# Performance work log

Measured on AMD Instinct MI355X. Metric: run time of the kernel, lower is better.

Reference implementation:

```python
import jax, jax.numpy as jnp
import numpy as np

B, D, E, K = 2048, 768, 8, 2   # tokens, d_model, num_experts, top-k
H = 4 * D                       # FeedForward hidden = 4 * n_embed
LOSS_COEF = 1e-2


def setup_inputs() -> dict:
    key = jax.random.key(0)
    ks = jax.random.split(key, 5)
    s = 0.02
    return {
        "x": jax.random.normal(ks[0], (B, D), jnp.float32),
        "w_gate": jax.random.normal(ks[1], (D, E), jnp.float32) * s,
        "W1": jax.random.normal(ks[2], (E, D, H), jnp.float32) * s,
        "b1": jnp.zeros((E, H), jnp.float32),
        "W2": jax.random.normal(ks[3], (E, H, D), jnp.float32) * s,
        "b2": jnp.zeros((E, D), jnp.float32),
    }


def _cv_squared(v):
    # torch .var() is unbiased (ddof=1)
    eps = 1e-10
    return v.var(ddof=1) / (v.mean() ** 2 + eps)


def reference(x, w_gate, W1, b1, W2, b2):
    # --- noisy_top_k_gating with train=False (clean logits, no noise) ---
    logits = x @ w_gate                                   # [B, E]
    top_vals, top_idx = jax.lax.top_k(logits, K)          # [B, K]
    top_gates = jax.nn.softmax(top_vals, axis=1)          # softmax over the k selected logits
    rows = jnp.arange(x.shape[0])[:, None]
    gates = jnp.zeros_like(logits).at[rows, top_idx].set(top_gates)  # scatter into [B, E]

    importance = gates.sum(0)                             # [E]
    load = (gates > 0).sum(0).astype(jnp.float32)         # [E] (_gates_to_load)
    loss = (_cv_squared(importance) + _cv_squared(load)) * LOSS_COEF

    # --- expert FFNs (dense over experts; gates zero out non-selected) ---
    # equivalent math to SparseDispatcher dispatch/compute/combine:
    # y[b] = sum_e gates[b,e] * FFN_e(x[b])
    h = jax.nn.gelu(jnp.einsum('bd,edh->ebh', x, W1) + b1[:, None, :], approximate=False)  # [E,B,H]
    out = jnp.einsum('ebh,ehd->ebd', h, W2) + b2[:, None, :]                               # [E,B,D]
    y = jnp.einsum('be,ebd->bd', gates, out)                                               # [B,D]
    return y, loss
```

## Files before the change

kernel.cpp:

```cpp
#include <hip/hip_runtime.h>
#include <math.h>

#define Btok 2048
#define Dm   768
#define NE   8
#define Hh   3072
#define OBROWS 5120

typedef short short8 __attribute__((ext_vector_type(8)));
typedef float f32x4  __attribute__((ext_vector_type(4)));

__device__ __forceinline__ short f2bf(float f) {
    unsigned u = __builtin_bit_cast(unsigned, f);
    u += 0x7fffu + ((u >> 16) & 1u);
    return (short)(u >> 16);
}

__device__ __forceinline__ float gelu_exact(float v) {
    return 0.5f * v * (1.0f + erff(v * 0.70710678118654752440f));
}

#define GLDS(gsrc, ldst)                                                           \
    __builtin_amdgcn_global_load_lds(                                              \
        (const __attribute__((address_space(1))) void*)(gsrc),                     \
        (__attribute__((address_space(3))) void*)(ldst),                           \
        16, 0, 0)

__device__ __forceinline__ void logits_body(const float* __restrict__ x,
                                            const float* __restrict__ wg,
                                            int* __restrict__ t2e,
                                            float* __restrict__ tokgate,
                                            unsigned short* __restrict__ xb,
                                            int b) {
    int wv   = threadIdx.x >> 6;
    int lane = threadIdx.x & 63;
    int tok  = b * 4 + wv;

    const float* xr = x + (size_t)tok * Dm;
    float xv[12];
#pragma unroll
    for (int i = 0; i < 12; ++i) xv[i] = xr[lane + i * 64];

    unsigned short* xw = xb + (size_t)tok * Dm;
#pragma unroll
    for (int i = 0; i < 12; ++i) xw[lane + i * 64] = (unsigned short)f2bf(xv[i]);

    float acc[NE];
#pragma unroll
    for (int e = 0; e < NE; ++e) acc[e] = 0.f;
#pragma unroll
    for (int i = 0; i < 12; ++i) {
        int d = lane + i * 64;
#pragma unroll
        for (int e = 0; e < NE; ++e) acc[e] += xv[i] * wg[d * NE + e];
    }
#pragma unroll
    for (int e = 0; e < NE; ++e) {
#pragma unroll
        for (int off = 32; off > 0; off >>= 1) acc[e] += __shfl_xor(acc[e], off);
    }

    if (lane == 0) {
        int i0 = 0; float v0 = acc[0];
#pragma unroll
        for (int e = 1; e < NE; ++e) { if (acc[e] > v0) { v0 = acc[e]; i0 = e; } }
        int i1 = -1; float v1 = -1e30f;
#pragma unroll
        for (int e = 0; e < NE; ++e) {
            if (e == i0) continue;
            if (acc[e] > v1) { v1 = acc[e]; i1 = e; }
        }
        float tt = __expf(v1 - v0);
        float g0 = 1.0f / (1.0f + tt);
        float g1 = 1.0f - g0;

        t2e[tok * 2 + 0]     = i0;
        t2e[tok * 2 + 1]     = i1;
        tokgate[tok * 2 + 0] = g0;
        tokgate[tok * 2 + 1] = g1;
    }
}

__device__ __forceinline__ void transpose_body(float (*tile)[65],
                                               const float* __restrict__ in,
                                               unsigned short* __restrict__ out,
                                               int ldIn, int ldOut,
                                               size_t eStrideIn, size_t eStrideOut,
                                               int rowOff, int colOff,
                                               int bx, int by, int bz) {
    const float* src = in + (size_t)bz * eStrideIn
                     + (size_t)(rowOff + by * 64) * ldIn + colOff + bx * 64;
    unsigned short* dst = out + (size_t)bz * eStrideOut
                        + (size_t)(bx * 64) * ldOut + by * 64;
    int t = threadIdx.x;
    int r = t >> 4, c4 = (t & 15) * 4;
#pragma unroll
    for (int it = 0; it < 4; ++it) {
        float4 v = *(const float4*)(src + (size_t)(it * 16 + r) * ldIn + c4);
        tile[it * 16 + r][c4 + 0] = v.x;
        tile[it * 16 + r][c4 + 1] = v.y;
        tile[it * 16 + r][c4 + 2] = v.z;
        tile[it * 16 + r][c4 + 3] = v.w;
    }
    __syncthreads();
#pragma unroll
    for (int it = 0; it < 4; ++it) {
        int n = it * 16 + r;
        unsigned short o0 = (unsigned short)f2bf(tile[c4 + 0][n]);
        unsigned short o1 = (unsigned short)f2bf(tile[c4 + 1][n]);
        unsigned short o2 = (unsigned short)f2bf(tile[c4 + 2][n]);
        unsigned short o3 = (unsigned short)f2bf(tile[c4 + 3][n]);
        uint2 o;
        o.x = (unsigned)o0 | ((unsigned)o1 << 16);
        o.y = (unsigned)o2 | ((unsigned)o3 << 16);
        *(uint2*)(dst + (size_t)n * ldOut + c4) = o;
    }
}

__global__ __launch_bounds__(256)
void transpose_kernel(const float* __restrict__ in, unsigned short* __restrict__ out,
                      int ldIn, int ldOut, size_t eStrideIn, size_t eStrideOut,
                      int rowOff, int colOff) {
    __shared__ float tile[64][65];
    transpose_body(tile, in, out, ldIn, ldOut, eStrideIn, eStrideOut, rowOff, colOff,
                   blockIdx.x, blockIdx.y, blockIdx.z);
}

__global__ __launch_bounds__(256)
void prep_kernel(const float* __restrict__ x,
                 const float* __restrict__ wg,
                 int* __restrict__ t2e,
                 float* __restrict__ tokgate,
                 unsigned short* __restrict__ xb,
                 const float* __restrict__ W1, unsigned short* __restrict__ w1t,
                 int Hc, int colBase) {
    __shared__ float tile[64][65];
    int b = blockIdx.x;
    const int NL = Btok / 4;

    if (b < NL) {
        logits_body(x, wg, t2e, tokgate, xb, b);
    } else {
        int nx1 = Hc / 64, ny1 = Dm / 64;
        int q  = b - NL;
        int bx = q % nx1; q /= nx1;
        int by = q % ny1;
        int bz = q / ny1;
        transpose_body(tile, W1, w1t, Hh, Dm, (size_t)Dm * Hh, (size_t)Hc * Dm,
                       0, colBase, bx, by, bz);
    }
}

__global__ __launch_bounds__(1024)
void assign_kernel(const int* __restrict__ t2e,
                   const float* __restrict__ tokgate,
                   int* __restrict__ padded,
                   int* __restrict__ offsets,
                   int* __restrict__ list,
                   int* __restrict__ tokes,
                   float* __restrict__ loss_out) {
    __shared__ int   scnt[NE];
    __shared__ int   spad[NE];
    __shared__ float simp[NE];
    int tid = threadIdx.x;
    if (tid < NE) { scnt[tid] = 0; simp[tid] = 0.f; }
    __syncthreads();

#pragma unroll
    for (int it = 0; it < Btok / 1024; ++it) {
        int tok = tid + it * 1024;
        int e0 = t2e[tok * 2], e1 = t2e[tok * 2 + 1];
        float g0 = tokgate[tok * 2], g1 = tokgate[tok * 2 + 1];
        int s0 = atomicAdd(&scnt[e0], 1);
        int s1 = atomicAdd(&scnt[e1], 1);
        list[e0 * Btok + s0] = tok;
        list[e1 * Btok + s1] = tok;
        tokes[tok * 2 + 0] = (e0 << 13) | s0;
        tokes[tok * 2 + 1] = (e1 << 13) | s1;
        atomicAdd(&simp[e0], g0);
        atomicAdd(&simp[e1], g1);
    }
    __syncthreads();

    if (tid == 0) {
        int off = 0;
        for (int e = 0; e < NE; ++e) {
            int p = (scnt[e] + 127) & ~127;
            spad[e]    = p;
            padded[e]  = p;
            offsets[e] = off;
            off += p;
        }
        float mi = 0.f, ml = 0.f;
        for (int e = 0; e < NE; ++e) { mi += simp[e]; ml += (float)scnt[e]; }
        mi *= (1.0f / NE); ml *= (1.0f / NE);
        float vi = 0.f, vl = 0.f;
        for (int e = 0; e < NE; ++e) {
            float di = simp[e] - mi;        vi += di * di;
            float dl = (float)scnt[e] - ml; vl += dl * dl;
        }
        vi /= (NE - 1); vl /= (NE - 1);
        loss_out[0] = 1e-2f * (vi / (mi * mi + 1e-10f) + vl / (ml * ml + 1e-10f));
    }
    __syncthreads();

    for (int e = 0; e < NE; ++e) {
        int c = scnt[e], p = spad[e];
        for (int s = c + tid; s < p; s += 1024) list[e * Btok + s] = 0;
    }
}

__global__ __launch_bounds__(256)
void gemm1_kernel(const unsigned short* __restrict__ xb,
                  const unsigned short* __restrict__ w1t,
                  const float* __restrict__ b1,
                  const int* __restrict__ list,
                  const int* __restrict__ padded,
                  const int* __restrict__ offsets,
                  unsigned short* __restrict__ hbuf,
                  int Hc, int colBase, int nG1, int nT2,
                  const float* __restrict__ W2,
                  unsigned short* __restrict__ w2t) {
    __shared__ union __align__(16) {
        struct { unsigned short As[2][4096]; unsigned short Bs[2][4096]; } g;
        float tile[64][65];
    } sm;

    int b = blockIdx.x;
    int gid;
    if (nT2 > 0) {
        int q = b / 5, r = b % 5;
        if (r >= 2) {
            int tix = q * 3 + (r - 2);
            int nx2 = Dm / 64, ny2 = Hc / 64;
            int bx = tix % nx2; tix /= nx2;
            int by = tix % ny2;
            int bz = tix / ny2;
            transpose_body(sm.tile, W2, w2t, Dm, Hc, (size_t)Hh * Dm, (size_t)Dm * Hc,
                           0, 0, bx, by, bz);
            return;
        }
        gid = q * 2 + r;
    } else {
        gid = b;
    }

    int NTQ = Hc / 128;
    int nt = gid % NTQ;
    int mt = (gid / NTQ) % 16;
    int e  = gid / (NTQ * 16);
    if (mt * 128 >= padded[e]) return;
    int roff = offsets[e];

    int t = threadIdx.x, w = t >> 6, lane = t & 63;
    int lr = lane & 15, lh = lane >> 4;
    int wr = (w >> 1) * 64, wc = (w & 1) * 64;
    int r0 = t >> 2;
    int ce = ((t & 3) ^ ((r0 >> 1) & 3)) * 8;
    int ks = (lh ^ ((lr >> 1) & 3)) * 8;

    const int* lst = list + e * Btok + mt * 128;
    int tok0 = lst[r0], tok1 = lst[64 + r0];
    const unsigned short* pa0 = xb + (size_t)tok0 * Dm + ce;
    const unsigned short* pa1 = xb + (size_t)tok1 * Dm + ce;
    const unsigned short* wbp = w1t + ((size_t)e * Hc + (size_t)nt * 128) * Dm;
    const unsigned short* pb0 = wbp + (size_t)r0 * Dm + ce;
    const unsigned short* pb1 = wbp + (size_t)(64 + r0) * Dm + ce;

    int s0 = __builtin_amdgcn_readfirstlane(w * 1024);

    f32x4 acc[4][4];
#pragma unroll
    for (int i = 0; i < 4; ++i)
#pragma unroll
        for (int j = 0; j < 4; ++j) acc[i][j] = (f32x4){0.f, 0.f, 0.f, 0.f};

    auto stage = [&](int buf, int kb) {
        GLDS(pa0 + kb, (char*)&sm.g.As[buf][0] + s0);
        GLDS(pa1 + kb, (char*)&sm.g.As[buf][0] + s0 + 4096);
        GLDS(pb0 + kb, (char*)&sm.g.Bs[buf][0] + s0);
        GLDS(pb1 + kb, (char*)&sm.g.Bs[buf][0] + s0 + 4096);
    };
    auto compute = [&](int buf) {
        short8 a[4], bq[4];
#pragma unroll
        for (int i = 0; i < 4; ++i) a[i] = *(const short8*)&sm.g.As[buf][(wr + i * 16 + lr) * 32 + ks];
#pragma unroll
        for (int j = 0; j < 4; ++j) bq[j] = *(const short8*)&sm.g.Bs[buf][(wc + j * 16 + lr) * 32 + ks];
#pragma unroll
        for (int i = 0; i < 4; ++i)
#pragma unroll
            for (int j = 0; j < 4; ++j)
                acc[i][j] = __builtin_amdgcn_mfma_f32_16x16x32_bf16(a[i], bq[j], acc[i][j], 0, 0, 0);
    };

    const int NTK = Dm / 32;
    stage(0, 0);
    __syncthreads();
    int cur = 0;
    for (int kt = 0; kt < NTK; ++kt) {
        if (kt + 1 < NTK) stage(cur ^ 1, (kt + 1) * 32);
        compute(cur);
        __syncthreads();
        cur ^= 1;
    }

    float bj[4];
#pragma unroll
    for (int j = 0; j < 4; ++j)
        bj[j] = b1[(size_t)e * Hh + colBase + nt * 128 + wc + j * 16 + lr];
#pragma unroll
    for (int i = 0; i < 4; ++i) {
#pragma unroll
        for (int j = 0; j < 4; ++j) {
#pragma unroll
            for (int r = 0; r < 4; ++r) {
                int row = wr + i * 16 + lh * 4 + r;
                float v = acc[i][j][r] + bj[j];
                v = gelu_exact(v);
                hbuf[(size_t)(roff + mt * 128 + row) * Hc + nt * 128 + wc + j * 16 + lr]
                    = (unsigned short)f2bf(v);
            }
        }
    }
}

__global__ __launch_bounds__(256)
void gemm2_kernel(const unsigned short* __restrict__ hbuf,
                  const unsigned short* __restrict__ w2t,
                  const int* __restrict__ padded,
                  const int* __restrict__ offsets,
                  float* __restrict__ obuf,
                  int Hc, int MT, int accum) {
    int id = blockIdx.x;
    int e  = id & 7;
    int rr = id >> 3;
    int mt = rr % MT; rr /= MT;
    int nt = rr % 6;
    int sk = rr / 6;
    if (mt * 128 >= padded[e]) return;
    int roff = offsets[e];
    int Kc = Hc >> 1, K0 = sk * Kc;

    __shared__ unsigned short As[2][4096];
    __shared__ unsigned short Bs[2][4096];

    int t = threadIdx.x, w = t >> 6, lane = t & 63;
    int lr = lane & 15, lh = lane >> 4;
    int wr = (w >> 1) * 64, wc = (w & 1) * 64;
    int r0 = t >> 2;
    int ce = ((t & 3) ^ ((r0 >> 1) & 3)) * 8;
    int ks = (lh ^ ((lr >> 1) & 3)) * 8;

    const unsigned short* ab  = hbuf + (size_t)(roff + mt * 128) * Hc + K0;
    const unsigned short* pa0 = ab + (size_t)r0 * Hc + ce;
    const unsigned short* pa1 = ab + (size_t)(64 + r0) * Hc + ce;
    const unsigned short* wbp = w2t + ((size_t)e * Dm + (size_t)nt * 128) * Hc + K0;
    const unsigned short* pb0 = wbp + (size_t)r0 * Hc + ce;
    const unsigned short* pb1 = wbp + (size_t)(64 + r0) * Hc + ce;

    int s0 = __builtin_amdgcn_readfirstlane(w * 1024);

    f32x4 acc[4][4];
#pragma unroll
    for (int i = 0; i < 4; ++i)
#pragma unroll
        for (int j = 0; j < 4; ++j) acc[i][j] = (f32x4){0.f, 0.f, 0.f, 0.f};

    auto stage = [&](int buf, int kb) {
        GLDS(pa0 + kb, (char*)&As[buf][0] + s0);
        GLDS(pa1 + kb, (char*)&As[buf][0] + s0 + 4096);
        GLDS(pb0 + kb, (char*)&Bs[buf][0] + s0);
        GLDS(pb1 + kb, (char*)&Bs[buf][0] + s0 + 4096);
    };
    auto compute = [&](int buf) {
        short8 a[4], bq[4];
#pragma unroll
        for (int i = 0; i < 4; ++i) a[i] = *(const short8*)&As[buf][(wr + i * 16 + lr) * 32 + ks];
#pragma unroll
        for (int j = 0; j < 4; ++j) bq[j] = *(const short8*)&Bs[buf][(wc + j * 16 + lr) * 32 + ks];
#pragma unroll
        for (int i = 0; i < 4; ++i)
#pragma unroll
            for (int j = 0; j < 4; ++j)
                acc[i][j] = __builtin_amdgcn_mfma_f32_16x16x32_bf16(a[i], bq[j], acc[i][j], 0, 0, 0);
    };

    const int NTK = Kc / 32;
    stage(0, 0);
    __syncthreads();
    int cur = 0;
    for (int kt = 0; kt < NTK; ++kt) {
        if (kt + 1 < NTK) stage(cur ^ 1, (kt + 1) * 32);
        compute(cur);
        __syncthreads();
        cur ^= 1;
    }

    float* orow = obuf + (size_t)sk * OBROWS * Dm
                + (size_t)(roff + mt * 128) * Dm + nt * 128;
#pragma unroll
    for (int i = 0; i < 4; ++i) {
#pragma unroll
        for (int r = 0; r < 4; ++r) {
            int row = wr + i * 16 + lh * 4 + r;
#pragma unroll
            for (int j = 0; j < 4; ++j) {
                int col = wc + j * 16 + lr;
                float v = acc[i][j][r];
                if (accum) v += orow[(size_t)row * Dm + col];
                orow[(size_t)row * Dm + col] = v;
            }
        }
    }
}

__global__ __launch_bounds__(256)
void combine_kernel(const float* __restrict__ obuf,
                    const int* __restrict__ offsets,
                    const int* __restrict__ tokes,
                    const float* __restrict__ tokgate,
                    const float* __restrict__ b2,
                    float* __restrict__ y) {
    int wv = threadIdx.x >> 6, lane = threadIdx.x & 63;
    int tok = blockIdx.x * 4 + wv;
    int p0 = tokes[tok * 2], p1 = tokes[tok * 2 + 1];
    float g0 = tokgate[tok * 2], g1 = tokgate[tok * 2 + 1];
    int e0 = p0 >> 13, ss0 = p0 & 8191;
    int e1 = p1 >> 13, ss1 = p1 & 8191;
    size_t r0 = (size_t)(offsets[e0] + ss0) * Dm;
    size_t r1 = (size_t)(offsets[e1] + ss1) * Dm;
    const size_t SLAB = (size_t)OBROWS * Dm;
#pragma unroll
    for (int i = 0; i < 3; ++i) {
        int col = (lane + i * 64) * 4;
        float4 a0 = *(const float4*)(obuf + r0 + col);
        float4 a1 = *(const float4*)(obuf + SLAB + r0 + col);
        float4 c0 = *(const float4*)(obuf + r1 + col);
        float4 c1 = *(const float4*)(obuf + SLAB + r1 + col);
        float4 be0 = *(const float4*)(b2 + (size_t)e0 * Dm + col);
        float4 be1 = *(const float4*)(b2 + (size_t)e1 * Dm + col);
        float4 o;
        o.x = g0 * (a0.x + a1.x + be0.x) + g1 * (c0.x + c1.x + be1.x);
        o.y = g0 * (a0.y + a1.y + be0.y) + g1 * (c0.y + c1.y + be1.y);
        o.z = g0 * (a0.z + a1.z + be0.z) + g1 * (c0.z + c1.z + be1.z);
        o.w = g0 * (a0.w + a1.w + be0.w) + g1 * (c0.w + c1.w + be1.w);
        *(float4*)(y + (size_t)tok * Dm + col) = o;
    }
}

extern "C" void kernel_launch(void* const* d_in, const int* in_sizes, int n_in,
                              void* d_out, int out_size, void* d_ws, size_t ws_size,
                              hipStream_t stream) {
    const float* x  = (const float*)d_in[0];
    const float* wg = (const float*)d_in[1];
    const float* W1 = (const float*)d_in[2];
    const float* b1 = (const float*)d_in[3];
    const float* W2 = (const float*)d_in[4];
    const float* b2 = (const float*)d_in[5];
    float* y = (float*)d_out;

    char* ws = (char*)d_ws;
    int*   padded     = (int*)(ws + 32);
    int*   offsets    = (int*)(ws + 64);
    int*   list       = (int*)(ws + 1024);
    int*   tokes      = (int*)(ws + 132096);
    float* tokgate    = (float*)(ws + 148480);
    int*   t2e        = (int*)(ws + 164864);
    unsigned short* xb = (unsigned short*)(ws + 262144);

    size_t base = (size_t)4 << 20;
    size_t osz  = (size_t)2 * OBROWS * Dm * sizeof(float);
    int C = 8;
    size_t wsz = 0, hsz = 0;
    for (int c = 1; c <= 8; c <<= 1) {
        wsz = (size_t)NE * (Hh / c) * Dm * 2;
        hsz = (size_t)OBROWS * (Hh / c) * 2;
        size_t need = base + 2 * wsz + hsz + ((c == 1) ? 0 : osz);
        C = c;
        if (need <= ws_size) break;
    }
    int Hc = Hh / C;
    wsz = (size_t)NE * Hc * Dm * 2;
    hsz = (size_t)OBROWS * Hc * 2;
    unsigned short* w1t  = (unsigned short*)(ws + base);
    unsigned short* w2t  = (unsigned short*)(ws + base + wsz);
    unsigned short* hbuf = (unsigned short*)(ws + base + 2 * wsz);
    float* obuf = (C == 1) ? (float*)w1t : (float*)(ws + base + 2 * wsz + hsz);

    const int MT = 16;
    int nT1 = (Hc / 64) * (Dm / 64) * NE;
    int nT2 = (Dm / 64) * (Hc / 64) * NE;
    int nG1 = (Hc / 128) * MT * NE;

    prep_kernel<<<Btok / 4 + nT1, 256, 0, stream>>>(
        x, wg, t2e, tokgate, xb, W1, w1t, Hc, 0);
    assign_kernel<<<1, 1024, 0, stream>>>(t2e, tokgate, padded, offsets, list, tokes,
                                          y + (size_t)Btok * Dm);

    for (int c = 0; c < C; ++c) {
        if (c > 0) {
            transpose_kernel<<<dim3(Hc / 64, Dm / 64, NE), 256, 0, stream>>>(
                W1, w1t, Hh, Dm, (size_t)Dm * Hh, (size_t)Hc * Dm, 0, c * Hc);
            transpose_kernel<<<dim3(Dm / 64, Hc / 64, NE), 256, 0, stream>>>(
                W2, w2t, Dm, Hc, (size_t)Hh * Dm, (size_t)Dm * Hc, c * Hc, 0);
        }
        int extra = (c == 0) ? nT2 : 0;
        gemm1_kernel<<<nG1 + extra, 256, 0, stream>>>(
            xb, w1t, b1, list, padded, offsets, hbuf, Hc, c * Hc, nG1, extra, W2, w2t);
        gemm2_kernel<<<8 * MT * 6 * 2, 256, 0, stream>>>(
            hbuf, w2t, padded, offsets, obuf, Hc, MT, (c == 0) ? 0 : 1);
    }
    combine_kernel<<<Btok / 4, 256, 0, stream>>>(obuf, offsets, tokes, tokgate, b2, y);
}
```

Baseline: 137.1 us.

## Compact active GEMM1 tiles and balance W2 transposes through an atomic queue

The assign kernel now builds a compact table of the non-empty (expert, row-tile) pairs and a tile count. GEMM1 blocks index into that table instead of mapping onto a fixed 16-tiles-per-expert grid, so blocks are no longer spent on tiles that immediately exit. The fused W2 transpose work is no longer statically given to 3 of every 5 blocks. Every block, including those that finish their GEMM tile, pulls transpose tiles from an atomic counter, which balances transpose work against GEMM work. The cost is an atomic plus two barriers per transpose tile, and the grid is now sized to nG1 with half its blocks doing only transposes in the first chunk.

Result: slower. 201.2 us (+46.7%).

```diff
diff --git a/kernel.cpp b/kernel.cpp
--- a/kernel.cpp
+++ b/kernel.cpp
@@ -158,7 +158,10 @@
                    int* __restrict__ offsets,
                    int* __restrict__ list,
                    int* __restrict__ tokes,
-                   float* __restrict__ loss_out) {
+                   float* __restrict__ loss_out,
+                   int* __restrict__ tbl,
+                   int* __restrict__ ntile,
+                   int* __restrict__ tq) {
     __shared__ int   scnt[NE];
     __shared__ int   spad[NE];
     __shared__ float simp[NE];
@@ -184,13 +187,17 @@
 
     if (tid == 0) {
         int off = 0;
+        int n = 0;
         for (int e = 0; e < NE; ++e) {
             int p = (scnt[e] + 127) & ~127;
             spad[e]    = p;
             padded[e]  = p;
             offsets[e] = off;
             off += p;
-        }
+            for (int mt = 0; mt * 128 < p; ++mt) tbl[n++] = (e << 8) | mt;
+        }
+        ntile[0] = n;
+        tq[0]    = 0;
         float mi = 0.f, ml = 0.f;
         for (int e = 0; e < NE; ++e) { mi += simp[e]; ml += (float)scnt[e]; }
         mi *= (1.0f / NE); ml *= (1.0f / NE);
@@ -215,112 +222,125 @@
                   const unsigned short* __restrict__ w1t,
                   const float* __restrict__ b1,
                   const int* __restrict__ list,
-                  const int* __restrict__ padded,
                   const int* __restrict__ offsets,
+                  const int* __restrict__ tbl,
+                  const int* __restrict__ ntile,
                   unsigned short* __restrict__ hbuf,
-                  int Hc, int colBase, int nG1, int nT2,
+                  int Hc, int colBase, int nT2,
                   const float* __restrict__ W2,
-                  unsigned short* __restrict__ w2t) {
+                  unsigned short* __restrict__ w2t,
+                  int* __restrict__ tq) {
     __shared__ union __align__(16) {
         struct { unsigned short As[2][4096]; unsigned short Bs[2][4096]; } g;
         float tile[64][65];
     } sm;
-
-    int b = blockIdx.x;
+    __shared__ int curT;
+
+    int bid = blockIdx.x;
     int gid;
     if (nT2 > 0) {
-        int q = b / 5, r = b % 5;
-        if (r >= 2) {
-            int tix = q * 3 + (r - 2);
-            int nx2 = Dm / 64, ny2 = Hc / 64;
-            int bx = tix % nx2; tix /= nx2;
-            int by = tix % ny2;
-            int bz = tix / ny2;
+        int q = bid >> 2, r = bid & 3;
+        gid = (r < 2) ? (q * 2 + r) : -1;
+    } else {
+        gid = bid;
+    }
+
+    int NTQ  = Hc / 128;
+    int nAct = ntile[0];
+
+    if (gid >= 0 && gid < nAct * NTQ) {
+        int nt = gid % NTQ;
+        int pk = tbl[gid / NTQ];
+        int e  = pk >> 8;
+        int mt = pk & 255;
+        int roff = offsets[e];
+
+        int t = threadIdx.x, w = t >> 6, lane = t & 63;
+        int lr = lane & 15, lh = lane >> 4;
+        int wr = (w >> 1) * 64, wc = (w & 1) * 64;
+        int r0 = t >> 2;
+        int ce = ((t & 3) ^ ((r0 >> 1) & 3)) * 8;
+        int ks = (lh ^ ((lr >> 1) & 3)) * 8;
+
+        const int* lst = list + e * Btok + mt * 128;
+        int tok0 = lst[r0], tok1 = lst[64 + r0];
+        const unsigned short* pa0 = xb + (size_t)tok0 * Dm + ce;
+        const unsigned short* pa1 = xb + (size_t)tok1 * Dm + ce;
+        const unsigned short* wbp = w1t + ((size_t)e * Hc + (size_t)nt * 128) * Dm;
+        const unsigned short* pb0 = wbp + (size_t)r0 * Dm + ce;
+        const unsigned short* pb1 = wbp + (size_t)(64 + r0) * Dm + ce;
+
+        int s0 = __builtin_amdgcn_readfirstlane(w * 1024);
+
+        f32x4 acc[4][4];
+#pragma unroll
+        for (int i = 0; i < 4; ++i)
+#pragma unroll
+            for (int j = 0; j < 4; ++j) acc[i][j] = (f32x4){0.f, 0.f, 0.f, 0.f};
+
+        auto stage = [&](int buf, int kb) {
+            GLDS(pa0 + kb, (char*)&sm.g.As[buf][0] + s0);
+            GLDS(pa1 + kb, (char*)&sm.g.As[buf][0] + s0 + 4096);
+            GLDS(pb0 + kb, (char*)&sm.g.Bs[buf][0] + s0);
+            GLDS(pb1 + kb, (char*)&sm.g.Bs[buf][0] + s0 + 4096);
+        };
+        auto compute = [&](int buf) {
+            short8 a[4], bq[4];
+#pragma unroll
+            for (int i = 0; i < 4; ++i) a[i] = *(const short8*)&sm.g.As[buf][(wr + i * 16 + lr) * 32 + ks];
+#pragma unroll
+            for (int j = 0; j < 4; ++j) bq[j] = *(const short8*)&sm.g.Bs[buf][(wc + j * 16 + lr) * 32 + ks];
+#pragma unroll
+            for (int i = 0; i < 4; ++i)
+#pragma unroll
+                for (int j = 0; j < 4; ++j)
+                    acc[i][j] = __builtin_amdgcn_mfma_f32_16x16x32_bf16(a[i], bq[j], acc[i][j], 0, 0, 0);
+        };
+
+        const int NTK = Dm / 32;
+        stage(0, 0);
+        __syncthreads();
+        int cur = 0;
+        for (int kt = 0; kt < NTK; ++kt) {
+            if (kt + 1 < NTK) stage(cur ^ 1, (kt + 1) * 32);
+            compute(cur);
+            __syncthreads();
+            cur ^= 1;
+        }
+
+        float bj[4];
+#pragma unroll
+        for (int j = 0; j < 4; ++j)
+            bj[j] = b1[(size_t)e * Hh + colBase + nt * 128 + wc + j * 16 + lr];
+#pragma unroll
+        for (int i = 0; i < 4; ++i) {
+#pragma unroll
+            for (int j = 0; j < 4; ++j) {
+#pragma unroll
+                for (int r = 0; r < 4; ++r) {
+                    int row = wr + i * 16 + lh * 4 + r;
+                    float v = acc[i][j][r] + bj[j];
+                    v = gelu_exact(v);
+                    hbuf[(size_t)(roff + mt * 128 + row) * Hc + nt * 128 + wc + j * 16 + lr]
+                        = (unsigned short)f2bf(v);
+                }
+            }
+        }
+    }
+
+    if (nT2 > 0) {
+        int nx2 = Dm / 64, ny2 = Hc / 64;
+        for (;;) {
+            __syncthreads();
+            if (threadIdx.x == 0) curT = atomicAdd(tq, 1);
+            __syncthreads();
+            int ti = curT;
+            if (ti >= nT2) break;
+            int bx = ti % nx2; int rem = ti / nx2;
+            int by = rem % ny2;
+            int bz = rem / ny2;
             transpose_body(sm.tile, W2, w2t, Dm, Hc, (size_t)Hh * Dm, (size_t)Dm * Hc,
                            0, 0, bx, by, bz);
-            return;
-        }
-        gid = q * 2 + r;
-    } else {
-        gid = b;
-    }
-
-    int NTQ = Hc / 128;
-    int nt = gid % NTQ;
-    int mt = (gid / NTQ) % 16;
-    int e  = gid / (NTQ * 16);
-    if (mt * 128 >= padded[e]) return;
-    int roff = offsets[e];
-
-    int t = threadIdx.x, w = t >> 6, lane = t & 63;
-    int lr = lane & 15, lh = lane >> 4;
-    int wr = (w >> 1) * 64, wc = (w & 1) * 64;
-    int r0 = t >> 2;
-    int ce = ((t & 3) ^ ((r0 >> 1) & 3)) * 8;
-    int ks = (lh ^ ((lr >> 1) & 3)) * 8;
-
-    const int* lst = list + e * Btok + mt * 128;
-    int tok0 = lst[r0], tok1 = lst[64 + r0];
-    const unsigned short* pa0 = xb + (size_t)tok0 * Dm + ce;
-    const unsigned short* pa1 = xb + (size_t)tok1 * Dm + ce;
-    const unsigned short* wbp = w1t + ((size_t)e * Hc + (size_t)nt * 128) * Dm;
-    const unsigned short* pb0 = wbp + (size_t)r0 * Dm + ce;
-    const unsigned short* pb1 = wbp + (size_t)(64 + r0) * Dm + ce;
-
-    int s0 = __builtin_amdgcn_readfirstlane(w * 1024);
-
-    f32x4 acc[4][4];
-#pragma unroll
-    for (int i = 0; i < 4; ++i)
-#pragma unroll
-        for (int j = 0; j < 4; ++j) acc[i][j] = (f32x4){0.f, 0.f, 0.f, 0.f};
-
-    auto stage = [&](int buf, int kb) {
-        GLDS(pa0 + kb, (char*)&sm.g.As[buf][0] + s0);
-        GLDS(pa1 + kb, (char*)&sm.g.As[buf][0] + s0 + 4096);
-        GLDS(pb0 + kb, (char*)&sm.g.Bs[buf][0] + s0);
-        GLDS(pb1 + kb, (char*)&sm.g.Bs[buf][0] + s0 + 4096);
-    };
-    auto compute = [&](int buf) {
-        short8 a[4], bq[4];
-#pragma unroll
-        for (int i = 0; i < 4; ++i) a[i] = *(const short8*)&sm.g.As[buf][(wr + i * 16 + lr) * 32 + ks];
-#pragma unroll
-        for (int j = 0; j < 4; ++j) bq[j] = *(const short8*)&sm.g.Bs[buf][(wc + j * 16 + lr) * 32 + ks];
-#pragma unroll
-        for (int i = 0; i < 4; ++i)
-#pragma unroll
-            for (int j = 0; j < 4; ++j)
-                acc[i][j] = __builtin_amdgcn_mfma_f32_16x16x32_bf16(a[i], bq[j], acc[i][j], 0, 0, 0);
-    };
-
-    const int NTK = Dm / 32;
-    stage(0, 0);
-    __syncthreads();
-    int cur = 0;
-    for (int kt = 0; kt < NTK; ++kt) {
-        if (kt + 1 < NTK) stage(cur ^ 1, (kt + 1) * 32);
-        compute(cur);
-        __syncthreads();
-        cur ^= 1;
-    }
-
-    float bj[4];
-#pragma unroll
-    for (int j = 0; j < 4; ++j)
-        bj[j] = b1[(size_t)e * Hh + colBase + nt * 128 + wc + j * 16 + lr];
-#pragma unroll
-    for (int i = 0; i < 4; ++i) {
-#pragma unroll
-        for (int j = 0; j < 4; ++j) {
-#pragma unroll
-            for (int r = 0; r < 4; ++r) {
-                int row = wr + i * 16 + lh * 4 + r;
-                float v = acc[i][j][r] + bj[j];
-                v = gelu_exact(v);
-                hbuf[(size_t)(roff + mt * 128 + row) * Hc + nt * 128 + wc + j * 16 + lr]
-                    = (unsigned short)f2bf(v);
-            }
         }
     }
 }
@@ -461,8 +481,11 @@
     float* y = (float*)d_out;
 
     char* ws = (char*)d_ws;
+    int*   tq         = (int*)(ws + 0);
+    int*   ntile      = (int*)(ws + 8);
     int*   padded     = (int*)(ws + 32);
     int*   offsets    = (int*)(ws + 64);
+    int*   tbl        = (int*)(ws + 96);
     int*   list       = (int*)(ws + 1024);
     int*   tokes      = (int*)(ws + 132096);
     float* tokgate    = (float*)(ws + 148480);
@@ -496,7 +519,7 @@
     prep_kernel<<<Btok / 4 + nT1, 256, 0, stream>>>(
         x, wg, t2e, tokgate, xb, W1, w1t, Hc, 0);
     assign_kernel<<<1, 1024, 0, stream>>>(t2e, tokgate, padded, offsets, list, tokes,
-                                          y + (size_t)Btok * Dm);
+                                          y + (size_t)Btok * Dm, tbl, ntile, tq);
 
     for (int c = 0; c < C; ++c) {
         if (c > 0) {
@@ -505,9 +528,9 @@
             transpose_kernel<<<dim3(Dm / 64, Hc / 64, NE), 256, 0, stream>>>(
                 W2, w2t, Dm, Hc, (size_t)Hh * Dm, (size_t)Dm * Hc, c * Hc, 0);
         }
-        int extra = (c == 0) ? nT2 : 0;
-        gemm1_kernel<<<nG1 + extra, 256, 0, stream>>>(
-            xb, w1t, b1, list, padded, offsets, hbuf, Hc, c * Hc, nG1, extra, W2, w2t);
+        gemm1_kernel<<<nG1, 256, 0, stream>>>(
+            xb, w1t, b1, list, offsets, tbl, ntile, hbuf, Hc, c * Hc,
+            (c == 0) ? nT2 : 0, W2, w2t, tq);
         gemm2_kernel<<<8 * MT * 6 * 2, 256, 0, stream>>>(
             hbuf, w2t, padded, offsets, obuf, Hc, MT, (c == 0) ? 0 : 1);
     }
```

## Move part of W2 transpose into the single-block assign kernel launch

Applied to the files above, without the earlier changes.

The assign kernel used to launch as one 1024-thread block, leaving most of the GPU idle. It now launches up to 2048 extra blocks that each transpose a 64x64 W2 tile to bf16 with a new 1024-thread transpose body. The remaining W2 tiles are spread evenly across the gemm1 grid by proportional indexing, replacing the fixed 2-of-5 interleave. The aim is to hide transpose work behind the latency-bound assign step and make gemm1 lighter. In exchange, the assign launch gets larger and its routing block may be scheduled alongside many transpose blocks.

Result: no change. 135.4 us (-1.2%).

```diff
diff --git a/kernel.cpp b/kernel.cpp
--- a/kernel.cpp
+++ b/kernel.cpp
@@ -117,6 +117,35 @@
     }
 }
 
+__device__ __forceinline__ void transpose_body_1k(float (*tile)[65],
+                                                  const float* __restrict__ in,
+                                                  unsigned short* __restrict__ out,
+                                                  int ldIn, int ldOut,
+                                                  size_t eStrideIn, size_t eStrideOut,
+                                                  int rowOff, int colOff,
+                                                  int bx, int by, int bz) {
+    const float* src = in + (size_t)bz * eStrideIn
+                     + (size_t)(rowOff + by * 64) * ldIn + colOff + bx * 64;
+    unsigned short* dst = out + (size_t)bz * eStrideOut
+                        + (size_t)(bx * 64) * ldOut + by * 64;
+    int t = threadIdx.x;
+    int r = t >> 4, c4 = (t & 15) * 4;
+    float4 v = *(const float4*)(src + (size_t)r * ldIn + c4);
+    tile[r][c4 + 0] = v.x;
+    tile[r][c4 + 1] = v.y;
+    tile[r][c4 + 2] = v.z;
+    tile[r][c4 + 3] = v.w;
+    __syncthreads();
+    unsigned short o0 = (unsigned short)f2bf(tile[c4 + 0][r]);
+    unsigned short o1 = (unsigned short)f2bf(tile[c4 + 1][r]);
+    unsigned short o2 = (unsigned short)f2bf(tile[c4 + 2][r]);
+    unsigned short o3 = (unsigned short)f2bf(tile[c4 + 3][r]);
+    uint2 o;
+    o.x = (unsigned)o0 | ((unsigned)o1 << 16);
+    o.y = (unsigned)o2 | ((unsigned)o3 << 16);
+    *(uint2*)(dst + (size_t)r * ldOut + c4) = o;
+}
+
 __global__ __launch_bounds__(256)
 void transpose_kernel(const float* __restrict__ in, unsigned short* __restrict__ out,
                       int ldIn, int ldOut, size_t eStrideIn, size_t eStrideOut,
@@ -158,10 +187,26 @@
                    int* __restrict__ offsets,
                    int* __restrict__ list,
                    int* __restrict__ tokes,
-                   float* __restrict__ loss_out) {
+                   float* __restrict__ loss_out,
+                   const float* __restrict__ W2,
+                   unsigned short* __restrict__ w2t,
+                   int Hc) {
     __shared__ int   scnt[NE];
     __shared__ int   spad[NE];
     __shared__ float simp[NE];
+    __shared__ float tile[64][65];
+
+    if (blockIdx.x > 0) {
+        int ti = blockIdx.x - 1;
+        int nx2 = Dm / 64, ny2 = Hc / 64;
+        int bx = ti % nx2; int q = ti / nx2;
+        int by = q % ny2;
+        int bz = q / ny2;
+        transpose_body_1k(tile, W2, w2t, Dm, Hc, (size_t)Hh * Dm, (size_t)Dm * Hc,
+                          0, 0, bx, by, bz);
+        return;
+    }
+
     int tid = threadIdx.x;
     if (tid < NE) { scnt[tid] = 0; simp[tid] = 0.f; }
     __syncthreads();
@@ -218,7 +263,7 @@
                   const int* __restrict__ padded,
                   const int* __restrict__ offsets,
                   unsigned short* __restrict__ hbuf,
-                  int Hc, int colBase, int nG1, int nT2,
+                  int Hc, int colBase, int nG1, int nTr, int tixBase,
                   const float* __restrict__ W2,
                   unsigned short* __restrict__ w2t) {
     __shared__ union __align__(16) {
@@ -228,19 +273,21 @@
 
     int b = blockIdx.x;
     int gid;
-    if (nT2 > 0) {
-        int q = b / 5, r = b % 5;
-        if (r >= 2) {
-            int tix = q * 3 + (r - 2);
+    if (nTr > 0) {
+        int total = nG1 + nTr;
+        int tc  = (int)(((long long)b * nTr) / total);
+        int tc1 = (int)(((long long)(b + 1) * nTr) / total);
+        if (tc1 != tc) {
+            int tix = tixBase + tc;
             int nx2 = Dm / 64, ny2 = Hc / 64;
-            int bx = tix % nx2; tix /= nx2;
-            int by = tix % ny2;
-            int bz = tix / ny2;
+            int bx = tix % nx2; int q = tix / nx2;
+            int by = q % ny2;
+            int bz = q / ny2;
             transpose_body(sm.tile, W2, w2t, Dm, Hc, (size_t)Hh * Dm, (size_t)Dm * Hc,
                            0, 0, bx, by, bz);
             return;
         }
-        gid = q * 2 + r;
+        gid = b - tc;
     } else {
         gid = b;
     }
@@ -493,10 +540,13 @@
     int nT2 = (Dm / 64) * (Hc / 64) * NE;
     int nG1 = (Hc / 128) * MT * NE;
 
+    int nTa = (nT2 < 2048) ? nT2 : 2048;
+    int nTr = nT2 - nTa;
+
     prep_kernel<<<Btok / 4 + nT1, 256, 0, stream>>>(
         x, wg, t2e, tokgate, xb, W1, w1t, Hc, 0);
-    assign_kernel<<<1, 1024, 0, stream>>>(t2e, tokgate, padded, offsets, list, tokes,
-                                          y + (size_t)Btok * Dm);
+    assign_kernel<<<1 + nTa, 1024, 0, stream>>>(t2e, tokgate, padded, offsets, list, tokes,
+                                                y + (size_t)Btok * Dm, W2, w2t, Hc);
 
     for (int c = 0; c < C; ++c) {
         if (c > 0) {
@@ -505,9 +555,9 @@
             transpose_kernel<<<dim3(Dm / 64, Hc / 64, NE), 256, 0, stream>>>(
                 W2, w2t, Dm, Hc, (size_t)Hh * Dm, (size_t)Dm * Hc, c * Hc, 0);
         }
-        int extra = (c == 0) ? nT2 : 0;
+        int extra = (c == 0) ? nTr : 0;
         gemm1_kernel<<<nG1 + extra, 256, 0, stream>>>(
-            xb, w1t, b1, list, padded, offsets, hbuf, Hc, c * Hc, nG1, extra, W2, w2t);
+            xb, w1t, b1, list, padded, offsets, hbuf, Hc, c * Hc, nG1, extra, nTa, W2, w2t);
         gemm2_kernel<<<8 * MT * 6 * 2, 256, 0, stream>>>(
             hbuf, w2t, padded, offsets, obuf, Hc, MT, (c == 0) ? 0 : 1);
     }
```
